# Optimization experiments

Measured on AMD Instinct MI355X. Metric: run time of the kernel, lower is better.

Reference implementation:

```python
import jax, jax.numpy as jnp
import numpy as np

B, N, E = 128, 100, 800          # graphs, nodes/graph, edges/graph
TN, TE = B * N, B * E
NODE_EMB, REL_EMB, H = 128, 256, 256   # hidden_size == relation_emb in CoMPILE
R, DEPTH = 200, 3
EDGE_EMB = 2 * NODE_EMB + REL_EMB      # 512


def _gru_dir(x, h0, w_ih, w_hh, b_ih, b_hh):
    """One direction of a torch-style GRU. x: [B,T,H], h0: [B,H] -> [B,T,H]."""
    def step(h, xt):
        gi = xt @ w_ih.T + b_ih
        gh = h @ w_hh.T + b_hh
        i_r, i_z, i_n = jnp.split(gi, 3, axis=-1)
        h_r, h_z, h_n = jnp.split(gh, 3, axis=-1)
        r = jax.nn.sigmoid(i_r + h_r)
        z = jax.nn.sigmoid(i_z + h_z)
        n = jnp.tanh(i_n + r * h_n)
        hn = (1.0 - z) * n + z * h
        return hn, hn
    _, ys = jax.lax.scan(step, h0, jnp.swapaxes(x, 0, 1))
    return jnp.swapaxes(ys, 0, 1)


def setup_inputs() -> dict:
    key = jax.random.key(0)
    ks = iter(jax.random.split(key, 40))
    def w(shape):
        return jax.random.normal(next(ks), shape, jnp.float32) * 0.05
    inp = {}
    inp["node_feat"] = jax.random.normal(next(ks), (TN, NODE_EMB), jnp.float32)
    inp["rel_emb"] = jax.random.normal(next(ks), (R, REL_EMB), jnp.float32)  # final_relation_embeddings
    # model weights (bias=False everywhere except W_o, linear1, gru)
    inp["W_i_node"] = w((H, NODE_EMB))
    inp["W_i_edge"] = w((H, EDGE_EMB))
    inp["Wa1"] = w((H, 2 * H))          # input_attention1
    inp["Wa2"] = w((1, H))              # input_attention2
    inp["W_h_atom"] = w((DEPTH - 1, H, H))
    inp["W_h_bond"] = w((DEPTH - 1, H, H))
    inp["Wd1"] = w((DEPTH - 1, H, H + REL_EMB))  # Attention1_d
    inp["Wd2"] = w((DEPTH - 1, 1, H))            # Attention2_d
    inp["W_comm"] = w((H, 3 * H))       # communicate_mlp
    inp["gru_bias"] = w((H,))
    inp["w_ih_f"] = w((3 * H, H)); inp["w_hh_f"] = w((3 * H, H))
    inp["b_ih_f"] = w((3 * H,));   inp["b_hh_f"] = w((3 * H,))
    inp["w_ih_b"] = w((3 * H, H)); inp["w_hh_b"] = w((3 * H, H))
    inp["b_ih_b"] = w((3 * H,));   inp["b_hh_b"] = w((3 * H,))
    inp["W_o"] = w((H, 2 * H)); inp["b_o"] = w((H,))
    inp["W_lin1"] = w((1, H)); inp["b_lin1"] = w((1,))
    # graph structure: edges stay inside their own subgraph (block-diagonal batching)
    off = (jnp.arange(B, dtype=jnp.int64)[:, None] * N)
    inp["edge_src"] = (jax.random.randint(next(ks), (B, E), 0, N) + off).reshape(-1)
    inp["edge_dst"] = (jax.random.randint(next(ks), (B, E), 0, N) + off).reshape(-1)
    inp["edge_rel"] = jax.random.randint(next(ks), (TE,), 0, R)
    inp["batch_rel"] = jax.random.randint(next(ks), (B,), 0, R)
    inp["src_node"] = jax.random.randint(next(ks), (B,), 0, N) + jnp.arange(B) * N
    inp["tgt_node"] = jax.random.randint(next(ks), (B,), 0, N) + jnp.arange(B) * N
    return inp


def reference(node_feat, rel_emb, W_i_node, W_i_edge, Wa1, Wa2, W_h_atom, W_h_bond,
              Wd1, Wd2, W_comm, gru_bias, w_ih_f, w_hh_f, b_ih_f, b_hh_f,
              w_ih_b, w_hh_b, b_ih_b, b_hh_b, W_o, b_o, W_lin1, b_lin1,
              edge_src, edge_dst, edge_rel, batch_rel, src_node, tgt_node):
    act = jax.nn.relu  # args.activation = 'ReLU'
    tgt_rel = rel_emb[batch_rel]                              # [B,H] per-query relation
    e_rel = rel_emb[edge_rel]                                 # [TE,H]
    edge_feat = jnp.concatenate([node_feat[edge_src], e_rel, node_feat[edge_dst]], 1)  # [TE,EDGE_EMB]
    input_node = act(node_feat @ W_i_node.T)                  # [TN,H]
    message_node = input_node
    input_edge = act(edge_feat @ W_i_edge.T)                  # [TE,H]
    message_edge = input_edge
    edge_tgt_rel = jnp.repeat(tgt_rel, E, axis=0)             # [TE,H] target relation per edge
    total_source = jnp.repeat(src_node, E)                    # [TE] query head node per edge
    total_target = jnp.repeat(tgt_node, E)
    # input edge attention vs translational query embedding
    g_edge = message_node[total_source] + edge_tgt_rel - message_node[total_target]
    att = jnp.tanh(jnp.concatenate([message_edge, g_edge], 1) @ Wa1.T)
    att = jax.nn.sigmoid(att @ Wa2.T)
    message_edge = message_edge * att
    for d in range(DEPTH - 1):
        # edge->node aggregation (MySpMM with target-side incidence e2n_sp)
        agg = jax.ops.segment_sum(message_edge, edge_dst, num_segments=TN)
        message_node = act((message_node + agg) @ W_h_atom[d].T)
        # node->edge (e2n_sp2^T: gather source-node states per edge)
        message_edge = act(input_edge + message_node[edge_src] @ W_h_bond[d].T)
        att = jnp.tanh(jnp.concatenate([message_edge, edge_tgt_rel], 1) @ Wd1[d].T)
        att = jax.nn.sigmoid(att @ Wd2[d].T)
        message_edge = message_edge * att
    agg = jax.ops.segment_sum(message_edge, edge_dst, num_segments=TN)
    agg2 = jnp.concatenate([agg, message_node, input_node], 1) @ W_comm.T  # [TN,H]
    # BatchGRU: uniform graph sizes -> pad/unpad is a reshape
    msg = act(agg2 + gru_bias).reshape(B, N, H)
    h0 = agg2.reshape(B, N, H).max(axis=1)                    # per-graph max of hidden
    out_f = _gru_dir(msg, h0, w_ih_f, w_hh_f, b_ih_f, b_hh_f)
    out_b = _gru_dir(msg[:, ::-1], h0, w_ih_b, w_hh_b, b_ih_b, b_hh_b)[:, ::-1]
    a_message = act(jnp.concatenate([out_f, out_b], -1).reshape(TN, 2 * H))
    atom_h = act(a_message @ W_o.T + b_o)                     # [TN,H]
    conv = jnp.tanh(atom_h[src_node] + tgt_rel - atom_h[tgt_node])  # [B,H]
    return conv @ W_lin1.T + b_lin1                           # [B,1]
```

## Files before the change

### kernel.cpp

```cpp
#include <hip/hip_runtime.h>
#include <cstddef>

#define Bg 128
#define Nn 100
#define Eg 800
#define TNODE 12800
#define TEDGE 102400
#define HD 256
#define NEMB 128
#define REMB 256

typedef short bf8 __attribute__((ext_vector_type(8)));
typedef short bf4 __attribute__((ext_vector_type(4)));
typedef float f4  __attribute__((ext_vector_type(4)));

__device__ __forceinline__ float relu_(float x){ return x > 0.f ? x : 0.f; }
__device__ __forceinline__ float sigm_(float x){ return 1.f/(1.f + __expf(-x)); }
__device__ __forceinline__ float4 ld4(const float* p){ return *(const float4*)p; }
__device__ __forceinline__ void st4(float* p, float4 v){ *(float4*)p = v; }
__device__ __forceinline__ float4 add4(float4 a, float4 b){
    return float4{a.x+b.x, a.y+b.y, a.z+b.z, a.w+b.w};
}
__device__ __forceinline__ float4 relu4(float4 a){
    return float4{relu_(a.x), relu_(a.y), relu_(a.z), relu_(a.w)};
}
__device__ __forceinline__ short f2bf(float f){
    unsigned u = __float_as_uint(f);
    u += 0x7fff + ((u >> 16) & 1);
    return (short)(u >> 16);
}
__device__ __forceinline__ float bf2f(short s){
    return __uint_as_float(((unsigned)(unsigned short)s) << 16);
}
__device__ __forceinline__ void split4(float4 v, bf4& h, bf4& l){
    h.x = f2bf(v.x); l.x = f2bf(v.x - bf2f(h.x));
    h.y = f2bf(v.y); l.y = f2bf(v.y - bf2f(h.y));
    h.z = f2bf(v.z); l.z = f2bf(v.z - bf2f(h.z));
    h.w = f2bf(v.w); l.w = f2bf(v.w - bf2f(h.w));
}
__device__ __forceinline__ f4 mfma_(bf8 a, bf8 b, f4 c){
    return __builtin_amdgcn_mfma_f32_16x16x32_bf16(a, b, c, 0, 0, 0);
}

enum { A_PLAIN=0, A_ADD=1, A_RELUB=2, A_CLAMP=3, A_CAT3=4, A_CAT2R=5 };
enum { E_STORE=0, E_RELU=1, E_BIAS=2, E_BIASRELU=3 };

template<int AM, int EM>
__global__ __launch_bounds__(256, 2)
void mgemm(const float* __restrict__ A0, const float* __restrict__ A1,
           const float* __restrict__ A2, const float* __restrict__ W,
           const float* __restrict__ bias, float* __restrict__ C,
           int M, int N, int K, int lda, int wld)
{
    __shared__ short Ah[128][40], Al[128][40], Bh[128][40], Bl[128][40];
    const int t  = threadIdx.x;
    const int kc = t & 7, lr = t >> 3;
    const int lane = t & 63, wv = t >> 6;
    const int wm = wv >> 1, wn = wv & 1;
    const int frow = lane & 15, fk = (lane >> 4) * 8;
    const int row0 = blockIdx.y * 128, col0 = blockIdx.x * 128;

    f4 acc[4][4] = {};

    for (int k0 = 0; k0 < K; k0 += 32) {
        const int gk = k0 + kc * 4;
        const int kk = kc * 4;
        #pragma unroll
        for (int ri = 0; ri < 4; ri++) {
            int row = lr + 32 * ri;
            int grow = row0 + row;
            float4 v;
            if (AM == A_PLAIN) {
                v = ld4(A0 + (size_t)grow * lda + gk);
            } else if (AM == A_ADD) {
                v = add4(ld4(A0 + (size_t)grow * lda + gk),
                         ld4(A1 + (size_t)grow * lda + gk));
            } else if (AM == A_RELUB) {
                v = relu4(add4(ld4(A0 + (size_t)grow * lda + gk), ld4(A1 + gk)));
            } else if (AM == A_CLAMP) {
                int cr = grow < M ? grow : M - 1;
                v = ld4(A0 + (size_t)cr * lda + gk);
            } else if (AM == A_CAT3) {
                if (gk < HD)        v = ld4(A0 + (size_t)grow * HD + gk);
                else if (gk < 2*HD) v = ld4(A1 + (size_t)grow * HD + gk - HD);
                else                v = ld4(A2 + (size_t)grow * HD + gk - 2*HD);
            } else {
                v = (gk < HD) ? relu4(ld4(A0 + (size_t)grow * HD + gk))
                              : relu4(ld4(A1 + (size_t)grow * HD + gk - HD));
            }
            bf4 h, l; split4(v, h, l);
            *(bf4*)&Ah[row][kk] = h;
            *(bf4*)&Al[row][kk] = l;
        }
        #pragma unroll
        for (int ri = 0; ri < 4; ri++) {
            int wr = lr + 32 * ri;
            float4 v = ld4(W + (size_t)(col0 + wr) * wld + gk);
            bf4 h, l; split4(v, h, l);
            *(bf4*)&Bh[wr][kk] = h;
            *(bf4*)&Bl[wr][kk] = l;
        }
        __syncthreads();
        bf8 ah[4], al[4], bh[4], bl[4];
        #pragma unroll
        for (int mi = 0; mi < 4; mi++) {
            ah[mi] = *(const bf8*)&Ah[wm*64 + mi*16 + frow][fk];
            al[mi] = *(const bf8*)&Al[wm*64 + mi*16 + frow][fk];
        }
        #pragma unroll
        for (int ni = 0; ni < 4; ni++) {
            bh[ni] = *(const bf8*)&Bh[wn*64 + ni*16 + frow][fk];
            bl[ni] = *(const bf8*)&Bl[wn*64 + ni*16 + frow][fk];
        }
        #pragma unroll
        for (int mi = 0; mi < 4; mi++)
            #pragma unroll
            for (int ni = 0; ni < 4; ni++) {
                acc[mi][ni] = mfma_(ah[mi], bh[ni], acc[mi][ni]);
                acc[mi][ni] = mfma_(ah[mi], bl[ni], acc[mi][ni]);
                acc[mi][ni] = mfma_(al[mi], bh[ni], acc[mi][ni]);
            }
        __syncthreads();
    }
    #pragma unroll
    for (int mi = 0; mi < 4; mi++) {
        #pragma unroll
        for (int ni = 0; ni < 4; ni++) {
            int ccol = col0 + wn*64 + ni*16 + frow;
            int rbase = row0 + wm*64 + mi*16 + (lane >> 4) * 4;
            #pragma unroll
            for (int reg = 0; reg < 4; reg++) {
                float v = acc[mi][ni][reg];
                if (EM == E_BIAS || EM == E_BIASRELU) v += bias[ccol];
                if (EM == E_RELU || EM == E_BIASRELU) v = relu_(v);
                C[(size_t)(rbase + reg) * N + ccol] = v;
            }
        }
    }
}

template<int MODE>
__global__ __launch_bounds__(256, 2)
void mattn(const float* __restrict__ S, const float* __restrict__ Rt,
           const float* __restrict__ D, const float* __restrict__ T0,
           const int* __restrict__ esrc, const int* __restrict__ erel,
           const int* __restrict__ edst,
           const float* __restrict__ W1, const float* __restrict__ W2,
           const float* __restrict__ term, float* __restrict__ sbuf)
{
    __shared__ short Ah[64][40], Al[64][40], Bh[256][40], Bl[256][40];
    __shared__ float partl[4][64];
    __shared__ int isrc[64], irel[64], idst[64];
    const int t = threadIdx.x;
    const int kc = t & 7, lr = t >> 3;
    const int lane = t & 63, wv = t >> 6;
    const int frow = lane & 15, fk = (lane >> 4) * 8;
    const int r0 = blockIdx.x * 64;

    if (t < 64) {
        int e = r0 + t;
        isrc[t] = esrc[e]; irel[t] = erel[e]; idst[t] = edst[e];
    }
    __syncthreads();

    f4 acc[4][4] = {};

    for (int k0 = 0; k0 < HD; k0 += 32) {
        const int gk = k0 + kc * 4;
        const int kk = kc * 4;
        #pragma unroll
        for (int ri = 0; ri < 2; ri++) {
            int row = lr + 32 * ri;
            int s = isrc[row], rl = irel[row], dd = idst[row];
            float4 v = relu4(add4(add4(ld4(S + (size_t)s * HD + gk),
                                       ld4(Rt + (size_t)rl * HD + gk)),
                                  ld4(D + (size_t)dd * HD + gk)));
            if (MODE) v = relu4(add4(v, ld4(T0 + (size_t)s * HD + gk)));
            bf4 h, l; split4(v, h, l);
            *(bf4*)&Ah[row][kk] = h;
            *(bf4*)&Al[row][kk] = l;
        }
        #pragma unroll
        for (int ri = 0; ri < 8; ri++) {
            int wr = lr + 32 * ri;
            float4 v = ld4(W1 + (size_t)wr * 512 + gk);
            bf4 h, l; split4(v, h, l);
            *(bf4*)&Bh[wr][kk] = h;
            *(bf4*)&Bl[wr][kk] = l;
        }
        __syncthreads();
        bf8 ah[4], al[4], bh[4], bl[4];
        #pragma unroll
        for (int mi = 0; mi < 4; mi++) {
            ah[mi] = *(const bf8*)&Ah[mi*16 + frow][fk];
            al[mi] = *(const bf8*)&Al[mi*16 + frow][fk];
        }
        #pragma unroll
        for (int ni = 0; ni < 4; ni++) {
            bh[ni] = *(const bf8*)&Bh[wv*64 + ni*16 + frow][fk];
            bl[ni] = *(const bf8*)&Bl[wv*64 + ni*16 + frow][fk];
        }
        #pragma unroll
        for (int mi = 0; mi < 4; mi++)
            #pragma unroll
            for (int ni = 0; ni < 4; ni++) {
                acc[mi][ni] = mfma_(ah[mi], bh[ni], acc[mi][ni]);
                acc[mi][ni] = mfma_(ah[mi], bl[ni], acc[mi][ni]);
                acc[mi][ni] = mfma_(al[mi], bh[ni], acc[mi][ni]);
            }
        __syncthreads();
    }
    #pragma unroll
    for (int mi = 0; mi < 4; mi++) {
        #pragma unroll
        for (int reg = 0; reg < 4; reg++) {
            int rl = mi*16 + (lane >> 4) * 4 + reg;
            int g = (r0 + rl) / Eg;
            float p = 0.f;
            #pragma unroll
            for (int ni = 0; ni < 4; ni++) {
                int n = wv*64 + ni*16 + frow;
                p += tanhf(acc[mi][ni][reg] + term[g*HD + n]) * W2[n];
            }
            p += __shfl_xor(p, 1); p += __shfl_xor(p, 2);
            p += __shfl_xor(p, 4); p += __shfl_xor(p, 8);
            if (frow == 0) partl[wv][rl] = p;
        }
    }
    __syncthreads();
    if (t < 64) {
        float p = partl[0][t] + partl[1][t] + partl[2][t] + partl[3][t];
        sbuf[r0 + t] = sigm_(p);
    }
}

template<int MODE>
__global__ __launch_bounds__(256)
void agg_gather(const float* __restrict__ S, const float* __restrict__ Rt,
                const float* __restrict__ D, const float* __restrict__ T0,
                const int* __restrict__ esrc, const int* __restrict__ erel,
                const int* __restrict__ rowptr, const int* __restrict__ eidx,
                const float* __restrict__ s, float* __restrict__ agg)
{
    int node = blockIdx.x * 4 + (threadIdx.x >> 6);
    int c = (threadIdx.x & 63) * 4;
    float4 dn = ld4(D + (size_t)node * HD + c);
    float4 acc{0.f, 0.f, 0.f, 0.f};
    int beg = rowptr[node], end = rowptr[node + 1];
    for (int i = beg; i < end; i++) {
        int e = eidx[i];
        int sr = esrc[e], rl = erel[e];
        float4 v = relu4(add4(add4(ld4(S + (size_t)sr * HD + c),
                                   ld4(Rt + (size_t)rl * HD + c)), dn));
        if (MODE) v = relu4(add4(v, ld4(T0 + (size_t)sr * HD + c)));
        float sc = s[e];
        acc.x += v.x * sc; acc.y += v.y * sc;
        acc.z += v.z * sc; acc.w += v.w * sc;
    }
    st4(agg + (size_t)node * HD + c, acc);
}

__global__ void zeroi_kernel(int* __restrict__ p)
{
    p[blockIdx.x * 256 + threadIdx.x] = 0;
}
__global__ void csr_count(const int* __restrict__ dst, int* __restrict__ cnt)
{
    int e = blockIdx.x * 256 + threadIdx.x;
    atomicAdd(&cnt[dst[e]], 1);
}
__global__ void csr_scan(const int* __restrict__ cnt, int* __restrict__ rowptr)
{
    __shared__ int ws[4];
    __shared__ int carry;
    int tid = threadIdx.x;
    if (tid == 0) carry = 0;
    __syncthreads();
    for (int i = 0; i < TNODE; i += 256) {
        int v = cnt[i + tid];
        int x = v;
        #pragma unroll
        for (int off = 1; off < 64; off <<= 1) {
            int y = __shfl_up(x, off);
            if ((tid & 63) >= off) x += y;
        }
        if ((tid & 63) == 63) ws[tid >> 6] = x;
        __syncthreads();
        int add = carry;
        int w = tid >> 6;
        for (int j = 0; j < w; j++) add += ws[j];
        rowptr[i + tid] = add + x - v;
        __syncthreads();
        if (tid == 255) carry = add + x;
        __syncthreads();
    }
    if (tid == 0) rowptr[TNODE] = carry;
}
__global__ void csr_fill(const int* __restrict__ dst, const int* __restrict__ rowptr,
                         int* __restrict__ fillc, int* __restrict__ eidx)
{
    int e = blockIdx.x * 256 + threadIdx.x;
    int d = dst[e];
    int slot = rowptr[d] + atomicAdd(&fillc[d], 1);
    eidx[slot] = e;
}

__global__ __launch_bounds__(256)
void term_kernel(const float* __restrict__ mn, const float* __restrict__ tgt_rel,
                 const float* __restrict__ Wa1, const float* __restrict__ Wd1,
                 const int* __restrict__ srcn, const int* __restrict__ tgtn,
                 float* __restrict__ term)
{
    __shared__ float Gs[HD];
    int b = blockIdx.x % Bg;
    int which = blockIdx.x / Bg;
    int c = threadIdx.x;
    float g;
    if (which == 0)
        g = mn[(size_t)srcn[b]*HD + c] + tgt_rel[b*HD + c] - mn[(size_t)tgtn[b]*HD + c];
    else
        g = tgt_rel[b*HD + c];
    Gs[c] = g;
    __syncthreads();
    const float* W = (which == 0) ? Wa1 : (Wd1 + (size_t)(which-1)*HD*512);
    float p = 0.f;
    for (int k = 0; k < HD; k += 4) {
        float4 w = ld4(W + (size_t)c*512 + 256 + k);
        p = fmaf(Gs[k], w.x, p); p = fmaf(Gs[k+1], w.y, p);
        p = fmaf(Gs[k+2], w.z, p); p = fmaf(Gs[k+3], w.w, p);
    }
    term[(size_t)which*Bg*HD + b*HD + c] = p;
}

__global__ void tgtrel_kernel(const float* __restrict__ rel_emb, const int* __restrict__ batch_rel,
                              float* __restrict__ tgt_rel)
{
    int b = blockIdx.x, c = threadIdx.x;
    tgt_rel[b*HD + c] = rel_emb[(size_t)batch_rel[b]*REMB + c];
}

__global__ void h0_kernel(const float* __restrict__ agg2, float* __restrict__ h0)
{
    int b = blockIdx.x, c = threadIdx.x;
    float m = -1e30f;
    for (int n = 0; n < Nn; n++)
        m = fmaxf(m, agg2[((size_t)b*Nn + n)*HD + c]);
    h0[b*HD + c] = m;
}

__global__ void whbf_kernel(const float* __restrict__ whf, const float* __restrict__ whb,
                            short* __restrict__ whbf)
{
    int idx = blockIdx.x * 256 + threadIdx.x;
    int d = idx / (768*256), rem = idx % (768*256);
    whbf[idx] = f2bf((d ? whb : whf)[rem]);
}

__global__ void biascomb_kernel(const float* __restrict__ bihf, const float* __restrict__ bhhf,
                                const float* __restrict__ bihb, const float* __restrict__ bhhb,
                                float* __restrict__ bc)
{
    int i = blockIdx.x * 256 + threadIdx.x;
    int d = i / 768, r = i % 768;
    const float* bi = d ? bihb : bihf;
    const float* bhh = d ? bhhb : bhhf;
    bc[i] = bi[r] + (r < 512 ? bhh[r] : 0.f);
}

__global__ __launch_bounds__(512, 2)
void gru_seq(const float* __restrict__ gi_f, const float* __restrict__ gi_b,
             const short* __restrict__ whbf,
             const float* __restrict__ bhf, const float* __restrict__ bhb,
             const float* __restrict__ h0,
             float* __restrict__ outf, float* __restrict__ outb)
{
    __shared__ float hsf[16][260];
    __shared__ short hsh[16][264];
    __shared__ short hsl[16][264];
    __shared__ float gates[768][17];
    const int blk = blockIdx.x;
    const int d = blk >> 3, grp = blk & 7;
    const int tid = threadIdx.x;
    const int lane = tid & 63, wv = tid >> 6;
    const int f16 = lane & 15;
    const int kb  = (lane >> 4) * 8;

    const short* wp0 = whbf + (size_t)d * 768 * 256;
    const float* gi  = d ? gi_b : gi_f;
    const float* bh  = d ? bhb : bhf;
    float* outp      = d ? outb : outf;

    bf8 wregA[3][8];
    #pragma unroll
    for (int j = 0; j < 3; j++) {
        int wr = (wv*6 + j) * 16 + f16;
        const short* wp = wp0 + (size_t)wr * 256 + kb;
        #pragma unroll
        for (int ks = 0; ks < 8; ks++)
            wregA[j][ks] = *(const bf8*)(wp + ks*32);
    }

    const int eseq = tid >> 5, ehb = tid & 31;
    float bhn[8];
    #pragma unroll
    for (int hh = 0; hh < 8; hh++) bhn[hh] = bh[512 + ehb + hh * 32];

    {
        #pragma unroll
        for (int hh = 0; hh < 8; hh++) {
            int h = ehb + hh * 32;
            float v = h0[(size_t)(grp*16 + eseq) * HD + h];
            hsf[eseq][h] = v;
            short hi = f2bf(v);
            hsh[eseq][h] = hi;
            hsl[eseq][h] = f2bf(v - bf2f(hi));
        }
    }
    __syncthreads();

    for (int t = 0; t < Nn; t++) {
        int trow = d ? (Nn - 1 - t) : t;
        float gr[8], gz[8], gn[8];
        {
            size_t girow = ((size_t)(grp*16 + eseq) * Nn + trow) * 768;
            #pragma unroll
            for (int hh = 0; hh < 8; hh++) {
                int h = ehb + hh * 32;
                gr[hh] = gi[girow + h];
                gz[hh] = gi[girow + 256 + h];
                gn[hh] = gi[girow + 512 + h];
            }
        }
        #pragma unroll
        for (int j = 0; j < 6; j++) {
            const short* wp = wp0 + (size_t)((wv*6 + j) * 16 + f16) * 256 + kb;
            f4 acc = {};
            #pragma unroll
            for (int ks = 0; ks < 8; ks++) {
                bf8 ahi = *(const bf8*)&hsh[f16][ks*32 + kb];
                bf8 alo = *(const bf8*)&hsl[f16][ks*32 + kb];
                bf8 b = (j < 3) ? wregA[j][ks] : *(const bf8*)(wp + ks*32);
                acc = mfma_(ahi, b, acc);
                acc = mfma_(alo, b, acc);
            }
            #pragma unroll
            for (int reg = 0; reg < 4; reg++)
                gates[(wv*6 + j)*16 + f16][(lane >> 4)*4 + reg] = acc[reg];
        }
        __syncthreads();
        {
            size_t orow = ((size_t)(grp*16 + eseq) * Nn + trow) * HD;
            #pragma unroll
            for (int hh = 0; hh < 8; hh++) {
                int h = ehb + hh * 32;
                float R  = gates[h][eseq];
                float Z  = gates[256 + h][eseq];
                float NN = gates[512 + h][eseq];
                float hprev = hsf[eseq][h];
                float r = sigm_(gr[hh] + R);
                float z = sigm_(gz[hh] + Z);
                float n = tanhf(gn[hh] + r * (NN + bhn[hh]));
                float nh = (1.f - z) * n + z * hprev;
                hsf[eseq][h] = nh;
                short hi = f2bf(nh);
                hsh[eseq][h] = hi;
                hsl[eseq][h] = f2bf(nh - bf2f(hi));
                outp[orow + h] = nh;
            }
        }
        __syncthreads();
    }
}

__global__ __launch_bounds__(256)
void final_kernel(const float* __restrict__ atom_h, const float* __restrict__ tgt_rel,
                  const int* __restrict__ srcn, const int* __restrict__ tgtn,
                  const float* __restrict__ Wl, const float* __restrict__ bl,
                  float* __restrict__ out)
{
    __shared__ float red[4];
    int b = blockIdx.x, c = threadIdx.x;
    float v = tanhf(atom_h[(size_t)srcn[b]*HD + c] + tgt_rel[b*HD + c]
                    - atom_h[(size_t)tgtn[b]*HD + c]);
    float p = v * Wl[c];
    #pragma unroll
    for (int off = 1; off < 64; off <<= 1) p += __shfl_xor(p, off);
    int wv = c >> 6;
    if ((c & 63) == 0) red[wv] = p;
    __syncthreads();
    if (c == 0) out[b] = red[0] + red[1] + red[2] + red[3] + bl[0];
}

extern "C" void kernel_launch(void* const* d_in, const int* in_sizes, int n_in,
                              void* d_out, int out_size, void* d_ws, size_t ws_size,
                              hipStream_t stream)
{
    const float* node_feat = (const float*)d_in[0];
    const float* rel_emb   = (const float*)d_in[1];
    const float* W_i_node  = (const float*)d_in[2];
    const float* W_i_edge  = (const float*)d_in[3];
    const float* Wa1       = (const float*)d_in[4];
    const float* Wa2       = (const float*)d_in[5];
    const float* W_h_atom  = (const float*)d_in[6];
    const float* W_h_bond  = (const float*)d_in[7];
    const float* Wd1       = (const float*)d_in[8];
    const float* Wd2       = (const float*)d_in[9];
    const float* W_comm    = (const float*)d_in[10];
    const float* gru_bias  = (const float*)d_in[11];
    const float* w_ih_f    = (const float*)d_in[12];
    const float* w_hh_f    = (const float*)d_in[13];
    const float* b_ih_f    = (const float*)d_in[14];
    const float* b_hh_f    = (const float*)d_in[15];
    const float* w_ih_b    = (const float*)d_in[16];
    const float* w_hh_b    = (const float*)d_in[17];
    const float* b_ih_b    = (const float*)d_in[18];
    const float* b_hh_b    = (const float*)d_in[19];
    const float* W_o       = (const float*)d_in[20];
    const float* b_o       = (const float*)d_in[21];
    const float* W_lin1    = (const float*)d_in[22];
    const float* b_lin1    = (const float*)d_in[23];
    const int* edge_src  = (const int*)d_in[24];
    const int* edge_dst  = (const int*)d_in[25];
    const int* edge_rel  = (const int*)d_in[26];
    const int* batch_rel = (const int*)d_in[27];
    const int* src_node  = (const int*)d_in[28];
    const int* tgt_node  = (const int*)d_in[29];
    float* out = (float*)d_out;

    float* ws = (float*)d_ws;
    size_t off = 0;
    auto alloc = [&](size_t n){ float* p = ws + off; off += n; return p; };
    float* tgt_rel    = alloc((size_t)Bg*HD);
    float* term       = alloc((size_t)3*Bg*HD);
    float* input_node = alloc((size_t)TNODE*HD);
    float* mn_a       = alloc((size_t)TNODE*HD);
    float* mn_b       = alloc((size_t)TNODE*HD);
    float* agg        = alloc((size_t)TNODE*HD);
    float* h0v        = alloc((size_t)Bg*HD);
    short* whbf       = (short*)alloc((size_t)2*768*256/2);
    float* bcomb      = alloc((size_t)2*768);
    float* sbuf       = alloc((size_t)TEDGE);
    int*   cnt        = (int*)alloc((size_t)TNODE);
    int*   fillc      = (int*)alloc((size_t)TNODE);
    int*   rowptr     = (int*)alloc((size_t)TNODE + 256);
    int*   eidx       = (int*)alloc((size_t)TEDGE);
    float* Sbuf       = alloc((size_t)TNODE*HD);
    float* Dbuf       = alloc((size_t)TNODE*HD);
    float* Rbuf       = alloc((size_t)256*HD);
    float* gi_f       = alloc((size_t)TNODE*768);
    float* gi_b       = alloc((size_t)TNODE*768);
    float* out_f      = alloc((size_t)TNODE*HD);
    float* out_b      = alloc((size_t)TNODE*HD);
    float* agg2   = mn_a;
    float* atom_h = input_node;

    tgtrel_kernel<<<Bg, 256, 0, stream>>>(rel_emb, batch_rel, tgt_rel);
    whbf_kernel<<<1536, 256, 0, stream>>>(w_hh_f, w_hh_b, whbf);
    biascomb_kernel<<<6, 256, 0, stream>>>(b_ih_f, b_hh_f, b_ih_b, b_hh_b, bcomb);

    zeroi_kernel<<<2*TNODE/256, 256, 0, stream>>>(cnt);
    csr_count<<<TEDGE/256, 256, 0, stream>>>(edge_dst, cnt);
    csr_scan<<<1, 256, 0, stream>>>(cnt, rowptr);
    csr_fill<<<TEDGE/256, 256, 0, stream>>>(edge_dst, rowptr, fillc, eidx);

    mgemm<A_PLAIN, E_RELU><<<dim3(HD/128, TNODE/128), 256, 0, stream>>>(
        node_feat, nullptr, nullptr, W_i_node, nullptr, input_node,
        TNODE, HD, NEMB, NEMB, NEMB);

    mgemm<A_PLAIN, E_STORE><<<dim3(HD/128, TNODE/128), 256, 0, stream>>>(
        node_feat, nullptr, nullptr, W_i_edge + 0, nullptr, Sbuf,
        TNODE, HD, NEMB, NEMB, 512);
    mgemm<A_PLAIN, E_STORE><<<dim3(HD/128, TNODE/128), 256, 0, stream>>>(
        node_feat, nullptr, nullptr, W_i_edge + 384, nullptr, Dbuf,
        TNODE, HD, NEMB, NEMB, 512);
    mgemm<A_CLAMP, E_STORE><<<dim3(HD/128, 2), 256, 0, stream>>>(
        rel_emb, nullptr, nullptr, W_i_edge + 128, nullptr, Rbuf,
        200, HD, REMB, REMB, 512);

    term_kernel<<<3*Bg, 256, 0, stream>>>(input_node, tgt_rel, Wa1, Wd1,
                                          src_node, tgt_node, term);

    mattn<0><<<TEDGE/64, 256, 0, stream>>>(Sbuf, Rbuf, Dbuf, Sbuf,
        edge_src, edge_rel, edge_dst, Wa1, Wa2, term, sbuf);
    agg_gather<0><<<TNODE/4, 256, 0, stream>>>(Sbuf, Rbuf, Dbuf, Sbuf,
        edge_src, edge_rel, rowptr, eidx, sbuf, agg);

    const float* mn_cur = input_node;
    float* bufs[2] = {mn_a, mn_b};
    for (int d = 0; d < 2; d++) {
        float* mn_next = bufs[d];
        float* tmp     = bufs[1-d];
        mgemm<A_ADD, E_RELU><<<dim3(2, TNODE/128), 256, 0, stream>>>(
            mn_cur, agg, nullptr, W_h_atom + (size_t)d*HD*HD, nullptr, mn_next,
            TNODE, HD, HD, HD, HD);
        mgemm<A_PLAIN, E_STORE><<<dim3(2, TNODE/128), 256, 0, stream>>>(
            mn_next, nullptr, nullptr, W_h_bond + (size_t)d*HD*HD, nullptr, tmp,
            TNODE, HD, HD, HD, HD);
        mattn<1><<<TEDGE/64, 256, 0, stream>>>(Sbuf, Rbuf, Dbuf, tmp,
            edge_src, edge_rel, edge_dst, Wd1 + (size_t)d*HD*512,
            Wd2 + (size_t)d*HD, term + (size_t)(1+d)*Bg*HD, sbuf);
        agg_gather<1><<<TNODE/4, 256, 0, stream>>>(Sbuf, Rbuf, Dbuf, tmp,
            edge_src, edge_rel, rowptr, eidx, sbuf, agg);
        mn_cur = mn_next;
    }

    mgemm<A_CAT3, E_STORE><<<dim3(2, TNODE/128), 256, 0, stream>>>(
        agg, (const float*)mn_cur, input_node, W_comm, nullptr, agg2,
        TNODE, HD, 3*HD, 0, 3*HD);

    h0_kernel<<<Bg, 256, 0, stream>>>(agg2, h0v);

    mgemm<A_RELUB, E_BIAS><<<dim3(768/128, TNODE/128), 256, 0, stream>>>(
        agg2, gru_bias, nullptr, w_ih_f, bcomb, gi_f,
        TNODE, 768, HD, HD, HD);
    mgemm<A_RELUB, E_BIAS><<<dim3(768/128, TNODE/128), 256, 0, stream>>>(
        agg2, gru_bias, nullptr, w_ih_b, bcomb + 768, gi_b,
        TNODE, 768, HD, HD, HD);

    gru_seq<<<16, 512, 0, stream>>>(gi_f, gi_b, whbf, b_hh_f, b_hh_b, h0v,
                                    out_f, out_b);

    mgemm<A_CAT2R, E_BIASRELU><<<dim3(2, TNODE/128), 256, 0, stream>>>(
        out_f, out_b, nullptr, W_o, b_o, atom_h,
        TNODE, HD, 2*HD, 0, 2*HD);

    final_kernel<<<Bg, 256, 0, stream>>>(atom_h, tgt_rel, src_node, tgt_node,
                                         W_lin1, b_lin1, out);
}
```

Baseline: 1.545 ms.

## Pre-split attention weights to bf16 hi/lo and enlarge mattn edge tile

A new prep kernel converts the attention weight matrices (Wa1 and both Wd1 slices) into bf16 high/low halves once, so mattn no longer re-splits the fp32 weights into shared memory on every block. mattn now processes 128 edges per block with 8x4 accumulator tiles and loads the pre-split weight fragments straight from global memory (L2-resident) instead of LDS, which doubles weight reuse per block and halves the grid. The GRU kernel also drops its register-cached copy of part of the recurrent weights and reloads them from global each step, likely to free registers. The risks are higher register pressure in mattn from the larger accumulator, and extra global loads in the GRU loop.

```diff
diff --git a/kernel.cpp b/kernel.cpp
--- a/kernel.cpp
+++ b/kernel.cpp
@@ -139,37 +139,51 @@
     }
 }
 
+__global__ void w1split_kernel(const float* __restrict__ Wa1, const float* __restrict__ Wd1,
+                               short* __restrict__ w1h, short* __restrict__ w1l)
+{
+    int idx = blockIdx.x * 256 + threadIdx.x;
+    int which = idx >> 16, rem = idx & 65535;
+    int r = rem >> 8, k = rem & 255;
+    const float* W = (which == 0) ? Wa1 : (Wd1 + (size_t)(which - 1) * 256 * 512);
+    float v = W[(size_t)r * 512 + k];
+    short hi = f2bf(v);
+    w1h[idx] = hi;
+    w1l[idx] = f2bf(v - bf2f(hi));
+}
+
 template<int MODE>
 __global__ __launch_bounds__(256, 2)
 void mattn(const float* __restrict__ S, const float* __restrict__ Rt,
            const float* __restrict__ D, const float* __restrict__ T0,
            const int* __restrict__ esrc, const int* __restrict__ erel,
            const int* __restrict__ edst,
-           const float* __restrict__ W1, const float* __restrict__ W2,
+           const short* __restrict__ w1h, const short* __restrict__ w1l,
+           const float* __restrict__ W2,
            const float* __restrict__ term, float* __restrict__ sbuf)
 {
-    __shared__ short Ah[64][40], Al[64][40], Bh[256][40], Bl[256][40];
-    __shared__ float partl[4][64];
-    __shared__ int isrc[64], irel[64], idst[64];
+    __shared__ short Ah[128][40], Al[128][40];
+    __shared__ float partl[4][128];
+    __shared__ int isrc[128], irel[128], idst[128];
     const int t = threadIdx.x;
     const int kc = t & 7, lr = t >> 3;
     const int lane = t & 63, wv = t >> 6;
-    const int frow = lane & 15, fk = (lane >> 4) * 8;
-    const int r0 = blockIdx.x * 64;
-
-    if (t < 64) {
+    const int frow = lane & 15, kb = (lane >> 4) * 8;
+    const int r0 = blockIdx.x * 128;
+
+    if (t < 128) {
         int e = r0 + t;
         isrc[t] = esrc[e]; irel[t] = erel[e]; idst[t] = edst[e];
     }
     __syncthreads();
 
-    f4 acc[4][4] = {};
-
-    for (int k0 = 0; k0 < HD; k0 += 32) {
-        const int gk = k0 + kc * 4;
+    f4 acc[8][4] = {};
+
+    for (int k0 = 0; k0 < 8; k0++) {
+        const int gk = k0 * 32 + kc * 4;
         const int kk = kc * 4;
         #pragma unroll
-        for (int ri = 0; ri < 2; ri++) {
+        for (int ri = 0; ri < 4; ri++) {
             int row = lr + 32 * ri;
             int s = isrc[row], rl = irel[row], dd = idst[row];
             float4 v = relu4(add4(add4(ld4(S + (size_t)s * HD + gk),
@@ -180,38 +194,31 @@
             *(bf4*)&Ah[row][kk] = h;
             *(bf4*)&Al[row][kk] = l;
         }
-        #pragma unroll
-        for (int ri = 0; ri < 8; ri++) {
-            int wr = lr + 32 * ri;
-            float4 v = ld4(W1 + (size_t)wr * 512 + gk);
-            bf4 h, l; split4(v, h, l);
-            *(bf4*)&Bh[wr][kk] = h;
-            *(bf4*)&Bl[wr][kk] = l;
-        }
-        __syncthreads();
-        bf8 ah[4], al[4], bh[4], bl[4];
-        #pragma unroll
-        for (int mi = 0; mi < 4; mi++) {
-            ah[mi] = *(const bf8*)&Ah[mi*16 + frow][fk];
-            al[mi] = *(const bf8*)&Al[mi*16 + frow][fk];
+        __syncthreads();
+        bf8 ah[8], al[8];
+        #pragma unroll
+        for (int mi = 0; mi < 8; mi++) {
+            ah[mi] = *(const bf8*)&Ah[mi*16 + frow][kb];
+            al[mi] = *(const bf8*)&Al[mi*16 + frow][kb];
         }
         #pragma unroll
         for (int ni = 0; ni < 4; ni++) {
-            bh[ni] = *(const bf8*)&Bh[wv*64 + ni*16 + frow][fk];
-            bl[ni] = *(const bf8*)&Bl[wv*64 + ni*16 + frow][fk];
-        }
-        #pragma unroll
-        for (int mi = 0; mi < 4; mi++)
-            #pragma unroll
-            for (int ni = 0; ni < 4; ni++) {
-                acc[mi][ni] = mfma_(ah[mi], bh[ni], acc[mi][ni]);
-                acc[mi][ni] = mfma_(ah[mi], bl[ni], acc[mi][ni]);
-                acc[mi][ni] = mfma_(al[mi], bh[ni], acc[mi][ni]);
-            }
+            int wr = wv*64 + ni*16 + frow;
+            const short* wp = (const short*)w1h + (size_t)wr * 256 + k0*32 + kb;
+            const short* lp = (const short*)w1l + (size_t)wr * 256 + k0*32 + kb;
+            bf8 bh = *(const bf8*)wp;
+            bf8 bl = *(const bf8*)lp;
+            #pragma unroll
+            for (int mi = 0; mi < 8; mi++) {
+                acc[mi][ni] = mfma_(ah[mi], bh, acc[mi][ni]);
+                acc[mi][ni] = mfma_(ah[mi], bl, acc[mi][ni]);
+                acc[mi][ni] = mfma_(al[mi], bh, acc[mi][ni]);
+            }
+        }
         __syncthreads();
     }
     #pragma unroll
-    for (int mi = 0; mi < 4; mi++) {
+    for (int mi = 0; mi < 8; mi++) {
         #pragma unroll
         for (int reg = 0; reg < 4; reg++) {
             int rl = mi*16 + (lane >> 4) * 4 + reg;
@@ -228,7 +235,7 @@
         }
     }
     __syncthreads();
-    if (t < 64) {
+    if (t < 128) {
         float p = partl[0][t] + partl[1][t] + partl[2][t] + partl[3][t];
         sbuf[r0 + t] = sigm_(p);
     }
@@ -390,16 +397,6 @@
     const float* bh  = d ? bhb : bhf;
     float* outp      = d ? outb : outf;
 
-    bf8 wregA[3][8];
-    #pragma unroll
-    for (int j = 0; j < 3; j++) {
-        int wr = (wv*6 + j) * 16 + f16;
-        const short* wp = wp0 + (size_t)wr * 256 + kb;
-        #pragma unroll
-        for (int ks = 0; ks < 8; ks++)
-            wregA[j][ks] = *(const bf8*)(wp + ks*32);
-    }
-
     const int eseq = tid >> 5, ehb = tid & 31;
     float bhn[8];
     #pragma unroll
@@ -433,13 +430,14 @@
         }
         #pragma unroll
         for (int j = 0; j < 6; j++) {
-            const short* wp = wp0 + (size_t)((wv*6 + j) * 16 + f16) * 256 + kb;
+            int wr = (wv*6 + j) * 16 + f16;
+            const short* wp = wp0 + (size_t)wr * 256 + kb;
             f4 acc = {};
             #pragma unroll
             for (int ks = 0; ks < 8; ks++) {
                 bf8 ahi = *(const bf8*)&hsh[f16][ks*32 + kb];
                 bf8 alo = *(const bf8*)&hsl[f16][ks*32 + kb];
-                bf8 b = (j < 3) ? wregA[j][ks] : *(const bf8*)(wp + ks*32);
+                bf8 b = *(const bf8*)(wp + ks*32);
                 acc = mfma_(ahi, b, acc);
                 acc = mfma_(alo, b, acc);
             }
@@ -538,6 +536,8 @@
     float* agg        = alloc((size_t)TNODE*HD);
     float* h0v        = alloc((size_t)Bg*HD);
     short* whbf       = (short*)alloc((size_t)2*768*256/2);
+    short* w1h        = (short*)alloc((size_t)3*256*256/2);
+    short* w1l        = (short*)alloc((size_t)3*256*256/2);
     float* bcomb      = alloc((size_t)2*768);
     float* sbuf       = alloc((size_t)TEDGE);
     int*   cnt        = (int*)alloc((size_t)TNODE);
@@ -556,6 +556,7 @@
 
     tgtrel_kernel<<<Bg, 256, 0, stream>>>(rel_emb, batch_rel, tgt_rel);
     whbf_kernel<<<1536, 256, 0, stream>>>(w_hh_f, w_hh_b, whbf);
+    w1split_kernel<<<768, 256, 0, stream>>>(Wa1, Wd1, w1h, w1l);
     biascomb_kernel<<<6, 256, 0, stream>>>(b_ih_f, b_hh_f, b_ih_b, b_hh_b, bcomb);
 
     zeroi_kernel<<<2*TNODE/256, 256, 0, stream>>>(cnt);
@@ -580,8 +581,8 @@
     term_kernel<<<3*Bg, 256, 0, stream>>>(input_node, tgt_rel, Wa1, Wd1,
                                           src_node, tgt_node, term);
 
-    mattn<0><<<TEDGE/64, 256, 0, stream>>>(Sbuf, Rbuf, Dbuf, Sbuf,
-        edge_src, edge_rel, edge_dst, Wa1, Wa2, term, sbuf);
+    mattn<0><<<TEDGE/128, 256, 0, stream>>>(Sbuf, Rbuf, Dbuf, Sbuf,
+        edge_src, edge_rel, edge_dst, w1h, w1l, Wa2, term, sbuf);
     agg_gather<0><<<TNODE/4, 256, 0, stream>>>(Sbuf, Rbuf, Dbuf, Sbuf,
         edge_src, edge_rel, rowptr, eidx, sbuf, agg);
 
@@ -596,9 +597,10 @@
         mgemm<A_PLAIN, E_STORE><<<dim3(2, TNODE/128), 256, 0, stream>>>(
             mn_next, nullptr, nullptr, W_h_bond + (size_t)d*HD*HD, nullptr, tmp,
             TNODE, HD, HD, HD, HD);
-        mattn<1><<<TEDGE/64, 256, 0, stream>>>(Sbuf, Rbuf, Dbuf, tmp,
-            edge_src, edge_rel, edge_dst, Wd1 + (size_t)d*HD*512,
-            Wd2 + (size_t)d*HD, term + (size_t)(1+d)*Bg*HD, sbuf);
+        mattn<1><<<TEDGE/128, 256, 0, stream>>>(Sbuf, Rbuf, Dbuf, tmp,
+            edge_src, edge_rel, edge_dst, w1h + (size_t)(1+d)*65536,
+            w1l + (size_t)(1+d)*65536, Wd2 + (size_t)d*HD,
+            term + (size_t)(1+d)*Bg*HD, sbuf);
         agg_gather<1><<<TNODE/4, 256, 0, stream>>>(Sbuf, Rbuf, Dbuf, tmp,
             edge_src, edge_rel, rowptr, eidx, sbuf, agg);
         mn_cur = mn_next;
```

Result: faster. 1.319 ms (-14.6%).
